# Performance work log

Hardware: AMD Instinct MI355X
Metric: run time of the kernel (lower is better)

Reference implementation:

```python
import jax, jax.numpy as jnp
import numpy as np

VOCAB = 4096
HIDDEN = 1024
BATCH = 64
SEQ = 256


def setup_inputs() -> dict:
    key = jax.random.key(0)
    ks = jax.random.split(key, 9)
    s = 0.02
    D = VOCAB + HIDDEN
    return {
        "X": jax.random.randint(ks[0], (BATCH, SEQ), 0, VOCAB),
        # gate weights stored as [in, out] = [VOCAB+HIDDEN, HIDDEN] (transposed torch Linear)
        "Wz": jax.random.normal(ks[1], (D, HIDDEN), dtype=jnp.float32) * s,
        "bz": jax.random.normal(ks[2], (HIDDEN,), dtype=jnp.float32) * s,
        "Wr": jax.random.normal(ks[3], (D, HIDDEN), dtype=jnp.float32) * s,
        "br": jax.random.normal(ks[4], (HIDDEN,), dtype=jnp.float32) * s,
        "Wh": jax.random.normal(ks[5], (D, HIDDEN), dtype=jnp.float32) * s,
        "bh": jax.random.normal(ks[6], (HIDDEN,), dtype=jnp.float32) * s,
        "Wo": jax.random.normal(ks[7], (HIDDEN, VOCAB), dtype=jnp.float32) * s,
        "bo": jax.random.normal(ks[8], (VOCAB,), dtype=jnp.float32) * s,
    }


def reference(X, Wz, bz, Wr, br, Wh, bh, Wo, bo):
    # X: [B, S] int tokens. torch does one_hot(X.T) -> time-major [S, B, V].
    # one_hot @ W_input_block == row gather of the input block of each gate weight.
    Xt = X.T  # [S, B]
    Wz_x, Wz_h = Wz[:VOCAB], Wz[VOCAB:]
    Wr_x, Wr_h = Wr[:VOCAB], Wr[VOCAB:]
    Wh_x, Wh_h = Wh[:VOCAB], Wh[VOCAB:]

    H0 = jnp.zeros((X.shape[0], HIDDEN), dtype=Wz.dtype)

    def step(H, x_t):
        # x_t: [B] int
        z = jax.nn.sigmoid(Wz_x[x_t] + H @ Wz_h + bz)
        r = jax.nn.sigmoid(Wr_x[x_t] + H @ Wr_h + br)
        h = jnp.tanh(Wh_x[x_t] + (r * H) @ Wh_h + bh)
        H_new = z * h + (1.0 - z) * H
        Y = H_new @ Wo + bo  # [B, V]
        return H_new, Y

    H_final, Ys = jax.lax.scan(step, H0, Xt)  # Ys: [S, B, V]
    # torch.cat(outputs, dim=0) over S tensors of [B, V] -> [S*B, V]
    out = Ys.reshape(-1, VOCAB)
    return out, (H_final,)
```

## Files before the change

### kernel.cpp

```cpp
#include <hip/hip_runtime.h>
#include <hip/hip_bf16.h>
#include <cstdint>
#include <cstddef>

#define VOCAB  4096
#define HIDDEN 1024
#define BATCH  64
#define SEQ    256
#define NWG    64

typedef __attribute__((ext_vector_type(8))) short short8;
typedef __attribute__((ext_vector_type(4))) float f32x4;

__device__ __forceinline__ unsigned short f2bf(float f) {
    union { float f; uint32_t u; } v; v.f = f;
    uint32_t u = v.u;
    u += 0x7FFFu + ((u >> 16) & 1u);
    return (unsigned short)(u >> 16);
}

__device__ __forceinline__ void ast16(unsigned short* p, unsigned short v) {
    __hip_atomic_store(p, v, __ATOMIC_RELAXED, __HIP_MEMORY_SCOPE_AGENT);
}

__device__ __forceinline__ short8 cld16(const unsigned short* p) {
    short8 v;
    asm volatile("global_load_dwordx4 %0, %1, off sc0 sc1"
                 : "=v"(v) : "v"(p) : "memory");
    return v;
}

__global__ __launch_bounds__(256) void k_zero(float* Hf, unsigned short* Hbf, int* flags) {
    int i = blockIdx.x * 256 + threadIdx.x;
    if (i < BATCH * HIDDEN) { Hf[i] = 0.f; Hbf[i] = 0; }
    if (i < NWG * 32) flags[i] = 0;
}

__global__ __launch_bounds__(256) void k_pack(const float* __restrict__ src,
                                              unsigned short* __restrict__ dst,
                                              int R, int C) {
    __shared__ float tile[32][33];
    int tilesC = C >> 5;
    int bx = blockIdx.x % tilesC;
    int by = blockIdx.x / tilesC;
    int tx = threadIdx.x & 31;
    int ty = threadIdx.x >> 5;
    int c0 = bx << 5, r0 = by << 5;
    #pragma unroll
    for (int s = 0; s < 4; ++s) {
        int r = ty + s * 8;
        tile[r][tx] = src[(size_t)(r0 + r) * C + (c0 + tx)];
    }
    __syncthreads();
    #pragma unroll
    for (int s = 0; s < 4; ++s) {
        int cc = ty + s * 8;
        dst[(size_t)(c0 + cc) * R + (r0 + tx)] = f2bf(tile[tx][cc]);
    }
}

__device__ __forceinline__ void flag_barrier(int* flags, int p) {
    asm volatile("s_waitcnt vmcnt(0)" ::: "memory");
    __syncthreads();
    if (threadIdx.x == 0)
        __hip_atomic_store(&flags[blockIdx.x * 32], p, __ATOMIC_RELAXED, __HIP_MEMORY_SCOPE_AGENT);
    if (threadIdx.x < NWG) {
        while (__hip_atomic_load(&flags[threadIdx.x * 32], __ATOMIC_RELAXED, __HIP_MEMORY_SCOPE_AGENT) < p)
            __builtin_amdgcn_s_sleep(1);
    }
    __syncthreads();
    __builtin_amdgcn_sched_barrier(0);
}

__global__ __launch_bounds__(256, 1) void k_scan(
    const int* __restrict__ X,
    const float* __restrict__ Wz, const float* __restrict__ bz,
    const float* __restrict__ Wr, const float* __restrict__ br,
    const float* __restrict__ Wh, const float* __restrict__ bh,
    const unsigned short* __restrict__ Wzh, const unsigned short* __restrict__ Wrh,
    const unsigned short* __restrict__ Whh,
    float* __restrict__ Hf, unsigned short* __restrict__ Hbf,
    unsigned short* __restrict__ rHbf, unsigned short* __restrict__ Hhist,
    int* __restrict__ flags)
{
    __shared__ __align__(16) unsigned short WzL[16 * 1024];
    __shared__ __align__(16) unsigned short WrL[16 * 1024];
    __shared__ __align__(16) unsigned short WhL[16 * 1024];

    const int tid  = threadIdx.x;
    const int g    = blockIdx.x;
    const int w    = tid >> 6;
    const int lane = tid & 63;
    const int row  = lane & 15;
    const int q    = lane >> 4;
    const int kq   = q << 3;
    const int col0 = g << 4;
    const int j    = col0 + row;
    const int b0   = w << 4;
    const int bq   = b0 + (q << 2);

    #pragma unroll
    for (int c = 0; c < 8; ++c) {
        int idx = tid + c * 256;
        int kkg = idx >> 6;
        int rem = idx & 63;
        int qq  = rem >> 4;
        int rr  = rem & 15;
        size_t srcoff = (size_t)(col0 + rr) * HIDDEN + kkg * 32 + qq * 8;
        *(short8*)&WzL[idx * 8] = *(const short8*)&Wzh[srcoff];
        *(short8*)&WrL[idx * 8] = *(const short8*)&Wrh[srcoff];
        *(short8*)&WhL[idx * 8] = *(const short8*)&Whh[srcoff];
    }
    __syncthreads();

    const float bzj = bz[j], brj = br[j], bhj = bh[j];

    float zreg[4] = {0.f, 0.f, 0.f, 0.f};
    float Hreg[4] = {0.f, 0.f, 0.f, 0.f};
    int p = 0;

    float ezc[4], erc[4], ehc[4];
    {
        int tk[4];
        #pragma unroll
        for (int r = 0; r < 4; ++r) tk[r] = X[(bq + r) * SEQ + 0];
        #pragma unroll
        for (int r = 0; r < 4; ++r) {
            ezc[r] = Wz[(size_t)tk[r] * HIDDEN + j];
            erc[r] = Wr[(size_t)tk[r] * HIDDEN + j];
            ehc[r] = Wh[(size_t)tk[r] * HIDDEN + j];
        }
    }

    for (int t = 0; t < SEQ; ++t) {
        const int tn = (t + 1 < SEQ) ? t + 1 : t;
        int tokn[4];
        float ezn[4], ern[4], ehn[4];

        {
            const unsigned short* ap = Hbf + (size_t)(b0 + row) * HIDDEN + kq;
            short8 A[32];
            #pragma unroll
            for (int kk = 0; kk < 32; ++kk)
                A[kk] = cld16(ap + kk * 32);
            #pragma unroll
            for (int r = 0; r < 4; ++r) {
                const int* px = X + (bq + r) * SEQ + tn;
                asm volatile("global_load_dword %0, %1, off" : "=v"(tokn[r]) : "v"(px) : "memory");
            }

            f32x4 accZ = {0.f, 0.f, 0.f, 0.f}, accR = {0.f, 0.f, 0.f, 0.f};
            asm volatile("s_waitcnt vmcnt(20)" ::: "memory");
            __builtin_amdgcn_sched_barrier(0);
            #pragma unroll
            for (int kk = 0; kk < 16; ++kk) {
                short8 bzf = *(const short8*)&WzL[kk * 512 + q * 128 + row * 8];
                short8 brf = *(const short8*)&WrL[kk * 512 + q * 128 + row * 8];
                accZ = __builtin_amdgcn_mfma_f32_16x16x32_bf16(A[kk], bzf, accZ, 0, 0, 0);
                accR = __builtin_amdgcn_mfma_f32_16x16x32_bf16(A[kk], brf, accR, 0, 0, 0);
            }
            asm volatile("s_waitcnt vmcnt(4)" ::: "memory");
            __builtin_amdgcn_sched_barrier(0);
            #pragma unroll
            for (int kk = 16; kk < 32; ++kk) {
                short8 bzf = *(const short8*)&WzL[kk * 512 + q * 128 + row * 8];
                short8 brf = *(const short8*)&WrL[kk * 512 + q * 128 + row * 8];
                accZ = __builtin_amdgcn_mfma_f32_16x16x32_bf16(A[kk], bzf, accZ, 0, 0, 0);
                accR = __builtin_amdgcn_mfma_f32_16x16x32_bf16(A[kk], brf, accR, 0, 0, 0);
            }
            #pragma unroll
            for (int r = 0; r < 4; ++r) {
                float rr = 1.f / (1.f + expf(-(accR[r] + erc[r] + brj)));
                ast16(&rHbf[(bq + r) * HIDDEN + j], f2bf(rr * Hreg[r]));
            }
            #pragma unroll
            for (int r = 0; r < 4; ++r)
                zreg[r] = 1.f / (1.f + expf(-(accZ[r] + ezc[r] + bzj)));
        }

        flag_barrier(flags, ++p);

        {
            const unsigned short* ap = rHbf + (size_t)(b0 + row) * HIDDEN + kq;
            short8 A[32];
            #pragma unroll
            for (int kk = 0; kk < 32; ++kk)
                A[kk] = cld16(ap + kk * 32);
            #pragma unroll
            for (int r = 0; r < 4; ++r) {
                const float* pz = Wz + (size_t)tokn[r] * HIDDEN + j;
                const float* pr = Wr + (size_t)tokn[r] * HIDDEN + j;
                const float* pm = Wh + (size_t)tokn[r] * HIDDEN + j;
                asm volatile("global_load_dword %0, %1, off" : "=v"(ezn[r]) : "v"(pz) : "memory");
                asm volatile("global_load_dword %0, %1, off" : "=v"(ern[r]) : "v"(pr) : "memory");
                asm volatile("global_load_dword %0, %1, off" : "=v"(ehn[r]) : "v"(pm) : "memory");
            }

            f32x4 accA = {0.f, 0.f, 0.f, 0.f}, accB = {0.f, 0.f, 0.f, 0.f};
            asm volatile("s_waitcnt vmcnt(28)" ::: "memory");
            __builtin_amdgcn_sched_barrier(0);
            #pragma unroll
            for (int kk = 0; kk < 16; ++kk) {
                short8 bf = *(const short8*)&WhL[kk * 512 + q * 128 + row * 8];
                if (kk & 1) accB = __builtin_amdgcn_mfma_f32_16x16x32_bf16(A[kk], bf, accB, 0, 0, 0);
                else        accA = __builtin_amdgcn_mfma_f32_16x16x32_bf16(A[kk], bf, accA, 0, 0, 0);
            }
            asm volatile("s_waitcnt vmcnt(12)" ::: "memory");
            __builtin_amdgcn_sched_barrier(0);
            #pragma unroll
            for (int kk = 16; kk < 32; ++kk) {
                short8 bf = *(const short8*)&WhL[kk * 512 + q * 128 + row * 8];
                if (kk & 1) accB = __builtin_amdgcn_mfma_f32_16x16x32_bf16(A[kk], bf, accB, 0, 0, 0);
                else        accA = __builtin_amdgcn_mfma_f32_16x16x32_bf16(A[kk], bf, accA, 0, 0, 0);
            }
            #pragma unroll
            for (int r = 0; r < 4; ++r) {
                int b = bq + r;
                float h  = tanhf(accA[r] + accB[r] + ehc[r] + bhj);
                float Hn = zreg[r] * h + (1.f - zreg[r]) * Hreg[r];
                Hreg[r] = Hn;
                unsigned short bfv = f2bf(Hn);
                ast16(&Hbf[b * HIDDEN + j], bfv);
                Hhist[(size_t)t * (BATCH * HIDDEN) + b * HIDDEN + j] = bfv;
                if (t == SEQ - 1) Hf[b * HIDDEN + j] = Hn;
            }
        }

        flag_barrier(flags, ++p);

        #pragma unroll
        for (int r = 0; r < 4; ++r) { ezc[r] = ezn[r]; erc[r] = ern[r]; ehc[r] = ehn[r]; }
    }
}

__global__ __launch_bounds__(256) void k_step1(
    const int* __restrict__ X,
    const float* __restrict__ Wz, const float* __restrict__ bz,
    const float* __restrict__ Wr, const float* __restrict__ br,
    const unsigned short* __restrict__ Wzh, const unsigned short* __restrict__ Wrh,
    const unsigned short* __restrict__ Hbf, const float* __restrict__ Hf,
    float* __restrict__ zbuf, unsigned short* __restrict__ rHbf, int t)
{
    int w    = threadIdx.x >> 6;
    int lane = threadIdx.x & 63;
    int nt = blockIdx.x;
    int mt = w;
    bool isz = nt < 64;
    const unsigned short* W = isz ? Wzh : Wrh;
    int ntl = nt & 63;
    int row = lane & 15;
    int kq  = (lane >> 4) << 3;
    const unsigned short* aptr = Hbf + (size_t)(mt * 16 + row) * HIDDEN + kq;
    const unsigned short* bptr = W   + (size_t)(ntl * 16 + row) * HIDDEN + kq;
    f32x4 acc = {0.f, 0.f, 0.f, 0.f};
    #pragma unroll 8
    for (int kk = 0; kk < HIDDEN / 32; ++kk) {
        short8 a = *(const short8*)(aptr + kk * 32);
        short8 b = *(const short8*)(bptr + kk * 32);
        acc = __builtin_amdgcn_mfma_f32_16x16x32_bf16(a, b, acc, 0, 0, 0);
    }
    int j = ntl * 16 + row;
    const float* Wemb = isz ? Wz : Wr;
    float bias = isz ? bz[j] : br[j];
    #pragma unroll
    for (int r = 0; r < 4; ++r) {
        int b = mt * 16 + ((lane >> 4) << 2) + r;
        int tok = X[b * SEQ + t];
        float pre = acc[r] + Wemb[(size_t)tok * HIDDEN + j] + bias;
        float s = 1.f / (1.f + expf(-pre));
        if (isz) zbuf[b * HIDDEN + j] = s;
        else     rHbf[b * HIDDEN + j] = f2bf(s * Hf[b * HIDDEN + j]);
    }
}

__global__ __launch_bounds__(256) void k_step2(
    const int* __restrict__ X,
    const float* __restrict__ Wh, const float* __restrict__ bh,
    const unsigned short* __restrict__ Whh,
    const unsigned short* __restrict__ rHbf,
    const float* __restrict__ zbuf,
    float* __restrict__ Hf, unsigned short* __restrict__ Hbf,
    unsigned short* __restrict__ Hhist, int t)
{
    int w    = threadIdx.x >> 6;
    int lane = threadIdx.x & 63;
    int nt = blockIdx.x;
    int mt = w;
    int row = lane & 15;
    int kq  = (lane >> 4) << 3;
    const unsigned short* aptr = rHbf + (size_t)(mt * 16 + row) * HIDDEN + kq;
    const unsigned short* bptr = Whh  + (size_t)(nt * 16 + row) * HIDDEN + kq;
    f32x4 acc = {0.f, 0.f, 0.f, 0.f};
    #pragma unroll 8
    for (int kk = 0; kk < HIDDEN / 32; ++kk) {
        short8 a = *(const short8*)(aptr + kk * 32);
        short8 b = *(const short8*)(bptr + kk * 32);
        acc = __builtin_amdgcn_mfma_f32_16x16x32_bf16(a, b, acc, 0, 0, 0);
    }
    int j = nt * 16 + row;
    float bias = bh[j];
    #pragma unroll
    for (int r = 0; r < 4; ++r) {
        int b = mt * 16 + ((lane >> 4) << 2) + r;
        int tok = X[b * SEQ + t];
        float pre = acc[r] + Wh[(size_t)tok * HIDDEN + j] + bias;
        float h = tanhf(pre);
        float z = zbuf[b * HIDDEN + j];
        float Hold = Hf[b * HIDDEN + j];
        float Hn = z * h + (1.f - z) * Hold;
        Hf[b * HIDDEN + j] = Hn;
        unsigned short bf = f2bf(Hn);
        Hbf[b * HIDDEN + j] = bf;
        Hhist[(size_t)t * (BATCH * HIDDEN) + b * HIDDEN + j] = bf;
    }
}

__global__ __launch_bounds__(256) void k_out(
    const unsigned short* __restrict__ A,
    const unsigned short* __restrict__ B,
    const float* __restrict__ bo,
    float* __restrict__ out)
{
    __shared__ __align__(16) unsigned short As[128 * 32];
    __shared__ __align__(16) unsigned short Bs[128 * 32];
    int bn = blockIdx.x & 31;
    int bm = blockIdx.x >> 5;
    int m0 = bm << 7, n0 = bn << 7;
    int tid  = threadIdx.x;
    int w    = tid >> 6, lane = tid & 63;
    int wm = w & 1, wn = w >> 1;
    int row = lane & 15;
    int kq  = (lane >> 4) << 3;

    f32x4 acc[4][4];
    #pragma unroll
    for (int i = 0; i < 4; ++i)
        #pragma unroll
        for (int jj = 0; jj < 4; ++jj)
            acc[i][jj] = (f32x4){0.f, 0.f, 0.f, 0.f};

    for (int k0 = 0; k0 < HIDDEN; k0 += 32) {
        #pragma unroll
        for (int c = 0; c < 2; ++c) {
            int off  = tid * 32 + c * 16;
            int rowi = off >> 6;
            int us   = (off & 63) >> 1;
            *(short8*)&As[rowi * 32 + us] =
                *(const short8*)&A[(size_t)(m0 + rowi) * HIDDEN + k0 + us];
            *(short8*)&Bs[rowi * 32 + us] =
                *(const short8*)&B[(size_t)(n0 + rowi) * HIDDEN + k0 + us];
        }
        __syncthreads();
        short8 a[4], b[4];
        #pragma unroll
        for (int i = 0; i < 4; ++i)
            a[i] = *(const short8*)&As[(wm * 64 + i * 16 + row) * 32 + kq];
        #pragma unroll
        for (int jj = 0; jj < 4; ++jj)
            b[jj] = *(const short8*)&Bs[(wn * 64 + jj * 16 + row) * 32 + kq];
        #pragma unroll
        for (int i = 0; i < 4; ++i)
            #pragma unroll
            for (int jj = 0; jj < 4; ++jj)
                acc[i][jj] = __builtin_amdgcn_mfma_f32_16x16x32_bf16(a[i], b[jj], acc[i][jj], 0, 0, 0);
        __syncthreads();
    }

    #pragma unroll
    for (int i = 0; i < 4; ++i) {
        #pragma unroll
        for (int jj = 0; jj < 4; ++jj) {
            int n = n0 + wn * 64 + jj * 16 + row;
            float bb = bo[n];
            #pragma unroll
            for (int r = 0; r < 4; ++r) {
                int m = m0 + wm * 64 + i * 16 + ((lane >> 4) << 2) + r;
                out[(size_t)m * VOCAB + n] = acc[i][jj][r] + bb;
            }
        }
    }
}

__global__ __launch_bounds__(256) void k_copyH(const float* __restrict__ Hf,
                                               float* __restrict__ out) {
    int i = blockIdx.x * 256 + threadIdx.x;
    if (i < BATCH * HIDDEN)
        out[(size_t)SEQ * BATCH * VOCAB + i] = Hf[i];
}

extern "C" void kernel_launch(void* const* d_in, const int* in_sizes, int n_in,
                              void* d_out, int out_size, void* d_ws, size_t ws_size,
                              hipStream_t stream) {
    const int*   X  = (const int*)  d_in[0];
    const float* Wz = (const float*)d_in[1];
    const float* bz = (const float*)d_in[2];
    const float* Wr = (const float*)d_in[3];
    const float* br = (const float*)d_in[4];
    const float* Wh = (const float*)d_in[5];
    const float* bh = (const float*)d_in[6];
    const float* Wo = (const float*)d_in[7];
    const float* bo = (const float*)d_in[8];
    float* out = (float*)d_out;
    char* ws = (char*)d_ws;

    float*          Hf    = (float*)(ws);
    float*          zbuf  = (float*)(ws + (256 << 10));
    int*            flags = (int*)(ws + (512 << 10));
    unsigned short* Hbf   = (unsigned short*)(ws + (528 << 10));
    unsigned short* rHbf  = (unsigned short*)(ws + (656 << 10));
    unsigned short* Wzh   = (unsigned short*)(ws + (1 << 20));
    unsigned short* Wrh   = Wzh + 1024 * 1024;
    unsigned short* Whh   = Wrh + 1024 * 1024;
    unsigned short* WoT   = Whh + 1024 * 1024;
    unsigned short* Hhist = WoT + (size_t)VOCAB * HIDDEN;

    k_zero<<<256, 256, 0, stream>>>(Hf, Hbf, flags);
    k_pack<<<32 * 32,  256, 0, stream>>>(Wz + (size_t)VOCAB * HIDDEN, Wzh, 1024, 1024);
    k_pack<<<32 * 32,  256, 0, stream>>>(Wr + (size_t)VOCAB * HIDDEN, Wrh, 1024, 1024);
    k_pack<<<32 * 32,  256, 0, stream>>>(Wh + (size_t)VOCAB * HIDDEN, Whh, 1024, 1024);
    k_pack<<<32 * 128, 256, 0, stream>>>(Wo, WoT, 1024, 4096);

    void* args[] = {
        (void*)&X, (void*)&Wz, (void*)&bz, (void*)&Wr, (void*)&br,
        (void*)&Wh, (void*)&bh, (void*)&Wzh, (void*)&Wrh, (void*)&Whh,
        (void*)&Hf, (void*)&Hbf, (void*)&rHbf, (void*)&Hhist, (void*)&flags
    };
    hipError_t cerr = hipLaunchCooperativeKernel((void*)k_scan, dim3(NWG), dim3(256),
                                                 args, 0, stream);
    if (cerr != hipSuccess) {
        for (int t = 0; t < SEQ; ++t) {
            k_step1<<<128, 256, 0, stream>>>(X, Wz, bz, Wr, br, Wzh, Wrh, Hbf, Hf, zbuf, rHbf, t);
            k_step2<<<64,  256, 0, stream>>>(X, Wh, bh, Whh, rHbf, zbuf, Hf, Hbf, Hhist, t);
        }
    }

    k_out<<<4096, 256, 0, stream>>>(Hhist, WoT, bo, out);
    k_copyH<<<256, 256, 0, stream>>>(Hf, out);
}
```

Before: 3.485 ms.

## Halve persistent scan workgroups, each owning 32 hidden columns

The persistent recurrent kernel now runs 32 workgroups instead of 64, each computing 32 hidden columns with two 16-column MFMA tiles per gate. This halves the number of participants in every cross-workgroup flag barrier and doubles MFMA work per wave. Because the z and r weights for 32 columns fill the LDS budget, the candidate-gate (Wh) weights are no longer staged in LDS and are read from global memory on every step. That trades lower barrier cost for more per-step global traffic, longer per-step compute, and less GPU occupancy.

```diff
diff --git a/kernel.cpp b/kernel.cpp
--- a/kernel.cpp
+++ b/kernel.cpp
@@ -7,7 +7,7 @@
 #define HIDDEN 1024
 #define BATCH  64
 #define SEQ    256
-#define NWG    64
+#define NWG    32
 
 typedef __attribute__((ext_vector_type(8))) short short8;
 typedef __attribute__((ext_vector_type(4))) float f32x4;
@@ -83,9 +83,8 @@
     unsigned short* __restrict__ rHbf, unsigned short* __restrict__ Hhist,
     int* __restrict__ flags)
 {
-    __shared__ __align__(16) unsigned short WzL[16 * 1024];
-    __shared__ __align__(16) unsigned short WrL[16 * 1024];
-    __shared__ __align__(16) unsigned short WhL[16 * 1024];
+    __shared__ __align__(16) unsigned short WzL[32 * 1024];
+    __shared__ __align__(16) unsigned short WrL[32 * 1024];
 
     const int tid  = threadIdx.x;
     const int g    = blockIdx.x;
@@ -94,48 +93,52 @@
     const int row  = lane & 15;
     const int q    = lane >> 4;
     const int kq   = q << 3;
-    const int col0 = g << 4;
-    const int j    = col0 + row;
+    const int col0 = g << 5;
+    const int j0   = col0 + row;
+    const int j1   = j0 + 16;
     const int b0   = w << 4;
     const int bq   = b0 + (q << 2);
 
     #pragma unroll
-    for (int c = 0; c < 8; ++c) {
+    for (int c = 0; c < 16; ++c) {
         int idx = tid + c * 256;
-        int kkg = idx >> 6;
-        int rem = idx & 63;
-        int qq  = rem >> 4;
-        int rr  = rem & 15;
-        size_t srcoff = (size_t)(col0 + rr) * HIDDEN + kkg * 32 + qq * 8;
-        *(short8*)&WzL[idx * 8] = *(const short8*)&Wzh[srcoff];
-        *(short8*)&WrL[idx * 8] = *(const short8*)&Wrh[srcoff];
-        *(short8*)&WhL[idx * 8] = *(const short8*)&Whh[srcoff];
+        int cb  = idx >> 11;
+        int kkg = (idx >> 6) & 31;
+        int qq  = (idx >> 4) & 3;
+        int rr  = idx & 15;
+        size_t so = (size_t)(col0 + cb * 16 + rr) * HIDDEN + kkg * 32 + qq * 8;
+        *(short8*)&WzL[idx * 8] = *(const short8*)&Wzh[so];
+        *(short8*)&WrL[idx * 8] = *(const short8*)&Wrh[so];
     }
     __syncthreads();
 
-    const float bzj = bz[j], brj = br[j], bhj = bh[j];
-
-    float zreg[4] = {0.f, 0.f, 0.f, 0.f};
-    float Hreg[4] = {0.f, 0.f, 0.f, 0.f};
+    const float bzj0 = bz[j0], bzj1 = bz[j1];
+    const float brj0 = br[j0], brj1 = br[j1];
+    const float bhj0 = bh[j0], bhj1 = bh[j1];
+
+    float zreg[2][4] = {};
+    float Hreg[2][4] = {};
     int p = 0;
 
-    float ezc[4], erc[4], ehc[4];
+    float ezc[2][4], erc[2][4], ehc[2][4];
     {
         int tk[4];
         #pragma unroll
         for (int r = 0; r < 4; ++r) tk[r] = X[(bq + r) * SEQ + 0];
         #pragma unroll
         for (int r = 0; r < 4; ++r) {
-            ezc[r] = Wz[(size_t)tk[r] * HIDDEN + j];
-            erc[r] = Wr[(size_t)tk[r] * HIDDEN + j];
-            ehc[r] = Wh[(size_t)tk[r] * HIDDEN + j];
+            size_t o0 = (size_t)tk[r] * HIDDEN + j0;
+            size_t o1 = (size_t)tk[r] * HIDDEN + j1;
+            ezc[0][r] = Wz[o0]; ezc[1][r] = Wz[o1];
+            erc[0][r] = Wr[o0]; erc[1][r] = Wr[o1];
+            ehc[0][r] = Wh[o0]; ehc[1][r] = Wh[o1];
         }
     }
 
     for (int t = 0; t < SEQ; ++t) {
         const int tn = (t + 1 < SEQ) ? t + 1 : t;
         int tokn[4];
-        float ezn[4], ern[4], ehn[4];
+        float ezn[2][4], ern[2][4], ehn[2][4];
 
         {
             const unsigned short* ap = Hbf + (size_t)(b0 + row) * HIDDEN + kq;
@@ -149,33 +152,45 @@
                 asm volatile("global_load_dword %0, %1, off" : "=v"(tokn[r]) : "v"(px) : "memory");
             }
 
-            f32x4 accZ = {0.f, 0.f, 0.f, 0.f}, accR = {0.f, 0.f, 0.f, 0.f};
+            f32x4 accZ0 = {0.f,0.f,0.f,0.f}, accZ1 = {0.f,0.f,0.f,0.f};
+            f32x4 accR0 = {0.f,0.f,0.f,0.f}, accR1 = {0.f,0.f,0.f,0.f};
             asm volatile("s_waitcnt vmcnt(20)" ::: "memory");
             __builtin_amdgcn_sched_barrier(0);
             #pragma unroll
             for (int kk = 0; kk < 16; ++kk) {
-                short8 bzf = *(const short8*)&WzL[kk * 512 + q * 128 + row * 8];
-                short8 brf = *(const short8*)&WrL[kk * 512 + q * 128 + row * 8];
-                accZ = __builtin_amdgcn_mfma_f32_16x16x32_bf16(A[kk], bzf, accZ, 0, 0, 0);
-                accR = __builtin_amdgcn_mfma_f32_16x16x32_bf16(A[kk], brf, accR, 0, 0, 0);
+                int lo = kk * 512 + q * 128 + row * 8;
+                short8 fz0 = *(const short8*)&WzL[lo];
+                short8 fz1 = *(const short8*)&WzL[16384 + lo];
+                short8 fr0 = *(const short8*)&WrL[lo];
+                short8 fr1 = *(const short8*)&WrL[16384 + lo];
+                accZ0 = __builtin_amdgcn_mfma_f32_16x16x32_bf16(A[kk], fz0, accZ0, 0, 0, 0);
+                accZ1 = __builtin_amdgcn_mfma_f32_16x16x32_bf16(A[kk], fz1, accZ1, 0, 0, 0);
+                accR0 = __builtin_amdgcn_mfma_f32_16x16x32_bf16(A[kk], fr0, accR0, 0, 0, 0);
+                accR1 = __builtin_amdgcn_mfma_f32_16x16x32_bf16(A[kk], fr1, accR1, 0, 0, 0);
             }
             asm volatile("s_waitcnt vmcnt(4)" ::: "memory");
             __builtin_amdgcn_sched_barrier(0);
             #pragma unroll
             for (int kk = 16; kk < 32; ++kk) {
-                short8 bzf = *(const short8*)&WzL[kk * 512 + q * 128 + row * 8];
-                short8 brf = *(const short8*)&WrL[kk * 512 + q * 128 + row * 8];
-                accZ = __builtin_amdgcn_mfma_f32_16x16x32_bf16(A[kk], bzf, accZ, 0, 0, 0);
-                accR = __builtin_amdgcn_mfma_f32_16x16x32_bf16(A[kk], brf, accR, 0, 0, 0);
+                int lo = kk * 512 + q * 128 + row * 8;
+                short8 fz0 = *(const short8*)&WzL[lo];
+                short8 fz1 = *(const short8*)&WzL[16384 + lo];
+                short8 fr0 = *(const short8*)&WrL[lo];
+                short8 fr1 = *(const short8*)&WrL[16384 + lo];
+                accZ0 = __builtin_amdgcn_mfma_f32_16x16x32_bf16(A[kk], fz0, accZ0, 0, 0, 0);
+                accZ1 = __builtin_amdgcn_mfma_f32_16x16x32_bf16(A[kk], fz1, accZ1, 0, 0, 0);
+                accR0 = __builtin_amdgcn_mfma_f32_16x16x32_bf16(A[kk], fr0, accR0, 0, 0, 0);
+                accR1 = __builtin_amdgcn_mfma_f32_16x16x32_bf16(A[kk], fr1, accR1, 0, 0, 0);
             }
             #pragma unroll
             for (int r = 0; r < 4; ++r) {
-                float rr = 1.f / (1.f + expf(-(accR[r] + erc[r] + brj)));
-                ast16(&rHbf[(bq + r) * HIDDEN + j], f2bf(rr * Hreg[r]));
-            }
-            #pragma unroll
-            for (int r = 0; r < 4; ++r)
-                zreg[r] = 1.f / (1.f + expf(-(accZ[r] + ezc[r] + bzj)));
+                float rv0 = 1.f / (1.f + expf(-(accR0[r] + erc[0][r] + brj0)));
+                float rv1 = 1.f / (1.f + expf(-(accR1[r] + erc[1][r] + brj1)));
+                ast16(&rHbf[(bq + r) * HIDDEN + j0], f2bf(rv0 * Hreg[0][r]));
+                ast16(&rHbf[(bq + r) * HIDDEN + j1], f2bf(rv1 * Hreg[1][r]));
+                zreg[0][r] = 1.f / (1.f + expf(-(accZ0[r] + ezc[0][r] + bzj0)));
+                zreg[1][r] = 1.f / (1.f + expf(-(accZ1[r] + ezc[1][r] + bzj1)));
+            }
         }
 
         flag_barrier(flags, ++p);
@@ -188,48 +203,57 @@
                 A[kk] = cld16(ap + kk * 32);
             #pragma unroll
             for (int r = 0; r < 4; ++r) {
-                const float* pz = Wz + (size_t)tokn[r] * HIDDEN + j;
-                const float* pr = Wr + (size_t)tokn[r] * HIDDEN + j;
-                const float* pm = Wh + (size_t)tokn[r] * HIDDEN + j;
-                asm volatile("global_load_dword %0, %1, off" : "=v"(ezn[r]) : "v"(pz) : "memory");
-                asm volatile("global_load_dword %0, %1, off" : "=v"(ern[r]) : "v"(pr) : "memory");
-                asm volatile("global_load_dword %0, %1, off" : "=v"(ehn[r]) : "v"(pm) : "memory");
-            }
-
-            f32x4 accA = {0.f, 0.f, 0.f, 0.f}, accB = {0.f, 0.f, 0.f, 0.f};
-            asm volatile("s_waitcnt vmcnt(28)" ::: "memory");
+                const float* pz0 = Wz + (size_t)tokn[r] * HIDDEN + j0;
+                const float* pz1 = Wz + (size_t)tokn[r] * HIDDEN + j1;
+                const float* pr0 = Wr + (size_t)tokn[r] * HIDDEN + j0;
+                const float* pr1 = Wr + (size_t)tokn[r] * HIDDEN + j1;
+                const float* pm0 = Wh + (size_t)tokn[r] * HIDDEN + j0;
+                const float* pm1 = Wh + (size_t)tokn[r] * HIDDEN + j1;
+                asm volatile("global_load_dword %0, %1, off" : "=v"(ezn[0][r]) : "v"(pz0) : "memory");
+                asm volatile("global_load_dword %0, %1, off" : "=v"(ezn[1][r]) : "v"(pz1) : "memory");
+                asm volatile("global_load_dword %0, %1, off" : "=v"(ern[0][r]) : "v"(pr0) : "memory");
+                asm volatile("global_load_dword %0, %1, off" : "=v"(ern[1][r]) : "v"(pr1) : "memory");
+                asm volatile("global_load_dword %0, %1, off" : "=v"(ehn[0][r]) : "v"(pm0) : "memory");
+                asm volatile("global_load_dword %0, %1, off" : "=v"(ehn[1][r]) : "v"(pm1) : "memory");
+            }
+
+            asm volatile("s_waitcnt vmcnt(24)" ::: "memory");
             __builtin_amdgcn_sched_barrier(0);
-            #pragma unroll
-            for (int kk = 0; kk < 16; ++kk) {
-                short8 bf = *(const short8*)&WhL[kk * 512 + q * 128 + row * 8];
-                if (kk & 1) accB = __builtin_amdgcn_mfma_f32_16x16x32_bf16(A[kk], bf, accB, 0, 0, 0);
-                else        accA = __builtin_amdgcn_mfma_f32_16x16x32_bf16(A[kk], bf, accA, 0, 0, 0);
-            }
-            asm volatile("s_waitcnt vmcnt(12)" ::: "memory");
-            __builtin_amdgcn_sched_barrier(0);
-            #pragma unroll
-            for (int kk = 16; kk < 32; ++kk) {
-                short8 bf = *(const short8*)&WhL[kk * 512 + q * 128 + row * 8];
-                if (kk & 1) accB = __builtin_amdgcn_mfma_f32_16x16x32_bf16(A[kk], bf, accB, 0, 0, 0);
-                else        accA = __builtin_amdgcn_mfma_f32_16x16x32_bf16(A[kk], bf, accA, 0, 0, 0);
+            const unsigned short* w0 = Whh + (size_t)j0 * HIDDEN + kq;
+            const unsigned short* w1 = Whh + (size_t)j1 * HIDDEN + kq;
+            f32x4 acc0 = {0.f,0.f,0.f,0.f}, acc1 = {0.f,0.f,0.f,0.f};
+            #pragma unroll
+            for (int kk = 0; kk < 32; ++kk) {
+                short8 fb0 = *(const short8*)(w0 + kk * 32);
+                short8 fb1 = *(const short8*)(w1 + kk * 32);
+                acc0 = __builtin_amdgcn_mfma_f32_16x16x32_bf16(A[kk], fb0, acc0, 0, 0, 0);
+                acc1 = __builtin_amdgcn_mfma_f32_16x16x32_bf16(A[kk], fb1, acc1, 0, 0, 0);
             }
             #pragma unroll
             for (int r = 0; r < 4; ++r) {
                 int b = bq + r;
-                float h  = tanhf(accA[r] + accB[r] + ehc[r] + bhj);
-                float Hn = zreg[r] * h + (1.f - zreg[r]) * Hreg[r];
-                Hreg[r] = Hn;
-                unsigned short bfv = f2bf(Hn);
-                ast16(&Hbf[b * HIDDEN + j], bfv);
-                Hhist[(size_t)t * (BATCH * HIDDEN) + b * HIDDEN + j] = bfv;
-                if (t == SEQ - 1) Hf[b * HIDDEN + j] = Hn;
+                float h0 = tanhf(acc0[r] + ehc[0][r] + bhj0);
+                float h1 = tanhf(acc1[r] + ehc[1][r] + bhj1);
+                float Hn0 = zreg[0][r] * h0 + (1.f - zreg[0][r]) * Hreg[0][r];
+                float Hn1 = zreg[1][r] * h1 + (1.f - zreg[1][r]) * Hreg[1][r];
+                Hreg[0][r] = Hn0; Hreg[1][r] = Hn1;
+                unsigned short v0 = f2bf(Hn0), v1 = f2bf(Hn1);
+                ast16(&Hbf[b * HIDDEN + j0], v0);
+                ast16(&Hbf[b * HIDDEN + j1], v1);
+                Hhist[(size_t)t * (BATCH * HIDDEN) + b * HIDDEN + j0] = v0;
+                Hhist[(size_t)t * (BATCH * HIDDEN) + b * HIDDEN + j1] = v1;
+                if (t == SEQ - 1) { Hf[b * HIDDEN + j0] = Hn0; Hf[b * HIDDEN + j1] = Hn1; }
             }
         }
 
         flag_barrier(flags, ++p);
 
         #pragma unroll
-        for (int r = 0; r < 4; ++r) { ezc[r] = ezn[r]; erc[r] = ern[r]; ehc[r] = ehn[r]; }
+        for (int r = 0; r < 4; ++r) {
+            ezc[0][r] = ezn[0][r]; ezc[1][r] = ezn[1][r];
+            erc[0][r] = ern[0][r]; erc[1][r] = ern[1][r];
+            ehc[0][r] = ehn[0][r]; ehc[1][r] = ehn[1][r];
+        }
     }
 }
 
```

Result: slower. 5.739 ms (+64.7%).

## Spread recurrent scan over 256 workgroups with split-K across waves

Applied to the files above, without the earlier changes.

The persistent scan kernel grows from 64 to 256 workgroups. Each one now owns a 16-column by 16-batch tile, and its four waves each take a quarter of the K dimension, summed through an LDS reduction. This shortens the serial MFMA chain and the per-wave H loads in every timestep, attacking the latency-bound recurrence. In exchange, the grid barrier now has to observe 256 flags, now packed contiguously instead of padded, and each step pays an extra workgroup sync for the reduction. It also relies on all 256 workgroups being co-resident.

```diff
diff --git a/kernel.cpp b/kernel.cpp
--- a/kernel.cpp
+++ b/kernel.cpp
@@ -7,7 +7,7 @@
 #define HIDDEN 1024
 #define BATCH  64
 #define SEQ    256
-#define NWG    64
+#define NWG    256
 
 typedef __attribute__((ext_vector_type(8))) short short8;
 typedef __attribute__((ext_vector_type(4))) float f32x4;
@@ -33,7 +33,7 @@
 __global__ __launch_bounds__(256) void k_zero(float* Hf, unsigned short* Hbf, int* flags) {
     int i = blockIdx.x * 256 + threadIdx.x;
     if (i < BATCH * HIDDEN) { Hf[i] = 0.f; Hbf[i] = 0; }
-    if (i < NWG * 32) flags[i] = 0;
+    if (i < 2048) flags[i] = 0;
 }
 
 __global__ __launch_bounds__(256) void k_pack(const float* __restrict__ src,
@@ -63,10 +63,17 @@
     asm volatile("s_waitcnt vmcnt(0)" ::: "memory");
     __syncthreads();
     if (threadIdx.x == 0)
-        __hip_atomic_store(&flags[blockIdx.x * 32], p, __ATOMIC_RELAXED, __HIP_MEMORY_SCOPE_AGENT);
-    if (threadIdx.x < NWG) {
-        while (__hip_atomic_load(&flags[threadIdx.x * 32], __ATOMIC_RELAXED, __HIP_MEMORY_SCOPE_AGENT) < p)
+        __hip_atomic_store(&flags[blockIdx.x], p, __ATOMIC_RELAXED, __HIP_MEMORY_SCOPE_AGENT);
+    if (threadIdx.x < 64) {
+        int l = threadIdx.x;
+        for (;;) {
+            int a = __hip_atomic_load(&flags[l],       __ATOMIC_RELAXED, __HIP_MEMORY_SCOPE_AGENT);
+            int b = __hip_atomic_load(&flags[64 + l],  __ATOMIC_RELAXED, __HIP_MEMORY_SCOPE_AGENT);
+            int c = __hip_atomic_load(&flags[128 + l], __ATOMIC_RELAXED, __HIP_MEMORY_SCOPE_AGENT);
+            int d = __hip_atomic_load(&flags[192 + l], __ATOMIC_RELAXED, __HIP_MEMORY_SCOPE_AGENT);
+            if (a >= p && b >= p && c >= p && d >= p) break;
             __builtin_amdgcn_s_sleep(1);
+        }
     }
     __syncthreads();
     __builtin_amdgcn_sched_barrier(0);
@@ -86,6 +93,8 @@
     __shared__ __align__(16) unsigned short WzL[16 * 1024];
     __shared__ __align__(16) unsigned short WrL[16 * 1024];
     __shared__ __align__(16) unsigned short WhL[16 * 1024];
+    __shared__ __align__(16) f32x4 redZ[4][64];
+    __shared__ __align__(16) f32x4 redR[4][64];
 
     const int tid  = threadIdx.x;
     const int g    = blockIdx.x;
@@ -94,9 +103,11 @@
     const int row  = lane & 15;
     const int q    = lane >> 4;
     const int kq   = q << 3;
-    const int col0 = g << 4;
+    const int cg   = g & 63;
+    const int bg   = g >> 6;
+    const int col0 = cg << 4;
+    const int b0   = bg << 4;
     const int j    = col0 + row;
-    const int b0   = w << 4;
     const int bq   = b0 + (q << 2);
 
     #pragma unroll
@@ -106,10 +117,10 @@
         int rem = idx & 63;
         int qq  = rem >> 4;
         int rr  = rem & 15;
-        size_t srcoff = (size_t)(col0 + rr) * HIDDEN + kkg * 32 + qq * 8;
-        *(short8*)&WzL[idx * 8] = *(const short8*)&Wzh[srcoff];
-        *(short8*)&WrL[idx * 8] = *(const short8*)&Wrh[srcoff];
-        *(short8*)&WhL[idx * 8] = *(const short8*)&Whh[srcoff];
+        size_t so = (size_t)(col0 + rr) * HIDDEN + kkg * 32 + qq * 8;
+        *(short8*)&WzL[idx * 8] = *(const short8*)&Wzh[so];
+        *(short8*)&WrL[idx * 8] = *(const short8*)&Wrh[so];
+        *(short8*)&WhL[idx * 8] = *(const short8*)&Whh[so];
     }
     __syncthreads();
 
@@ -139,53 +150,51 @@
 
         {
             const unsigned short* ap = Hbf + (size_t)(b0 + row) * HIDDEN + kq;
-            short8 A[32];
-            #pragma unroll
-            for (int kk = 0; kk < 32; ++kk)
-                A[kk] = cld16(ap + kk * 32);
+            short8 A[8];
+            #pragma unroll
+            for (int kkL = 0; kkL < 8; ++kkL)
+                A[kkL] = cld16(ap + (w * 8 + kkL) * 32);
             #pragma unroll
             for (int r = 0; r < 4; ++r) {
                 const int* px = X + (bq + r) * SEQ + tn;
                 asm volatile("global_load_dword %0, %1, off" : "=v"(tokn[r]) : "v"(px) : "memory");
             }
 
-            f32x4 accZ = {0.f, 0.f, 0.f, 0.f}, accR = {0.f, 0.f, 0.f, 0.f};
-            asm volatile("s_waitcnt vmcnt(20)" ::: "memory");
-            __builtin_amdgcn_sched_barrier(0);
-            #pragma unroll
-            for (int kk = 0; kk < 16; ++kk) {
-                short8 bzf = *(const short8*)&WzL[kk * 512 + q * 128 + row * 8];
-                short8 brf = *(const short8*)&WrL[kk * 512 + q * 128 + row * 8];
-                accZ = __builtin_amdgcn_mfma_f32_16x16x32_bf16(A[kk], bzf, accZ, 0, 0, 0);
-                accR = __builtin_amdgcn_mfma_f32_16x16x32_bf16(A[kk], brf, accR, 0, 0, 0);
-            }
+            f32x4 aZ = {0.f,0.f,0.f,0.f}, aR = {0.f,0.f,0.f,0.f};
             asm volatile("s_waitcnt vmcnt(4)" ::: "memory");
             __builtin_amdgcn_sched_barrier(0);
             #pragma unroll
-            for (int kk = 16; kk < 32; ++kk) {
-                short8 bzf = *(const short8*)&WzL[kk * 512 + q * 128 + row * 8];
-                short8 brf = *(const short8*)&WrL[kk * 512 + q * 128 + row * 8];
-                accZ = __builtin_amdgcn_mfma_f32_16x16x32_bf16(A[kk], bzf, accZ, 0, 0, 0);
-                accR = __builtin_amdgcn_mfma_f32_16x16x32_bf16(A[kk], brf, accR, 0, 0, 0);
-            }
+            for (int kkL = 0; kkL < 8; ++kkL) {
+                int lo = (w * 8 + kkL) * 512 + q * 128 + row * 8;
+                short8 fz = *(const short8*)&WzL[lo];
+                short8 fr = *(const short8*)&WrL[lo];
+                aZ = __builtin_amdgcn_mfma_f32_16x16x32_bf16(A[kkL], fz, aZ, 0, 0, 0);
+                aR = __builtin_amdgcn_mfma_f32_16x16x32_bf16(A[kkL], fr, aR, 0, 0, 0);
+            }
+            redZ[w][lane] = aZ;
+            redR[w][lane] = aR;
+            __syncthreads();
+            f32x4 sZ = redZ[0][lane]; f32x4 sR = redR[0][lane];
+            #pragma unroll
+            for (int ww = 1; ww < 4; ++ww) { sZ += redZ[ww][lane]; sR += redR[ww][lane]; }
+
             #pragma unroll
             for (int r = 0; r < 4; ++r) {
-                float rr = 1.f / (1.f + expf(-(accR[r] + erc[r] + brj)));
-                ast16(&rHbf[(bq + r) * HIDDEN + j], f2bf(rr * Hreg[r]));
-            }
-            #pragma unroll
-            for (int r = 0; r < 4; ++r)
-                zreg[r] = 1.f / (1.f + expf(-(accZ[r] + ezc[r] + bzj)));
+                float rv = 1.f / (1.f + expf(-(sR[r] + erc[r] + brj)));
+                zreg[r]  = 1.f / (1.f + expf(-(sZ[r] + ezc[r] + bzj)));
+                if (w == 0)
+                    ast16(&rHbf[(bq + r) * HIDDEN + j], f2bf(rv * Hreg[r]));
+            }
         }
 
         flag_barrier(flags, ++p);
 
         {
             const unsigned short* ap = rHbf + (size_t)(b0 + row) * HIDDEN + kq;
-            short8 A[32];
-            #pragma unroll
-            for (int kk = 0; kk < 32; ++kk)
-                A[kk] = cld16(ap + kk * 32);
+            short8 A[8];
+            #pragma unroll
+            for (int kkL = 0; kkL < 8; ++kkL)
+                A[kkL] = cld16(ap + (w * 8 + kkL) * 32);
             #pragma unroll
             for (int r = 0; r < 4; ++r) {
                 const float* pz = Wz + (size_t)tokn[r] * HIDDEN + j;
@@ -196,33 +205,33 @@
                 asm volatile("global_load_dword %0, %1, off" : "=v"(ehn[r]) : "v"(pm) : "memory");
             }
 
-            f32x4 accA = {0.f, 0.f, 0.f, 0.f}, accB = {0.f, 0.f, 0.f, 0.f};
-            asm volatile("s_waitcnt vmcnt(28)" ::: "memory");
-            __builtin_amdgcn_sched_barrier(0);
-            #pragma unroll
-            for (int kk = 0; kk < 16; ++kk) {
-                short8 bf = *(const short8*)&WhL[kk * 512 + q * 128 + row * 8];
-                if (kk & 1) accB = __builtin_amdgcn_mfma_f32_16x16x32_bf16(A[kk], bf, accB, 0, 0, 0);
-                else        accA = __builtin_amdgcn_mfma_f32_16x16x32_bf16(A[kk], bf, accA, 0, 0, 0);
-            }
+            f32x4 aH = {0.f,0.f,0.f,0.f};
             asm volatile("s_waitcnt vmcnt(12)" ::: "memory");
             __builtin_amdgcn_sched_barrier(0);
             #pragma unroll
-            for (int kk = 16; kk < 32; ++kk) {
-                short8 bf = *(const short8*)&WhL[kk * 512 + q * 128 + row * 8];
-                if (kk & 1) accB = __builtin_amdgcn_mfma_f32_16x16x32_bf16(A[kk], bf, accB, 0, 0, 0);
-                else        accA = __builtin_amdgcn_mfma_f32_16x16x32_bf16(A[kk], bf, accA, 0, 0, 0);
-            }
+            for (int kkL = 0; kkL < 8; ++kkL) {
+                int lo = (w * 8 + kkL) * 512 + q * 128 + row * 8;
+                short8 fh = *(const short8*)&WhL[lo];
+                aH = __builtin_amdgcn_mfma_f32_16x16x32_bf16(A[kkL], fh, aH, 0, 0, 0);
+            }
+            redZ[w][lane] = aH;
+            __syncthreads();
+            f32x4 sH = redZ[0][lane];
+            #pragma unroll
+            for (int ww = 1; ww < 4; ++ww) sH += redZ[ww][lane];
+
             #pragma unroll
             for (int r = 0; r < 4; ++r) {
                 int b = bq + r;
-                float h  = tanhf(accA[r] + accB[r] + ehc[r] + bhj);
+                float h  = tanhf(sH[r] + ehc[r] + bhj);
                 float Hn = zreg[r] * h + (1.f - zreg[r]) * Hreg[r];
                 Hreg[r] = Hn;
-                unsigned short bfv = f2bf(Hn);
-                ast16(&Hbf[b * HIDDEN + j], bfv);
-                Hhist[(size_t)t * (BATCH * HIDDEN) + b * HIDDEN + j] = bfv;
-                if (t == SEQ - 1) Hf[b * HIDDEN + j] = Hn;
+                if (w == 0) {
+                    unsigned short bfv = f2bf(Hn);
+                    ast16(&Hbf[b * HIDDEN + j], bfv);
+                    Hhist[(size_t)t * (BATCH * HIDDEN) + b * HIDDEN + j] = bfv;
+                    if (t == SEQ - 1) Hf[b * HIDDEN + j] = Hn;
+                }
             }
         }
 
```

Measured after the change: 3.558 ms. 1.02x slower.

## Split recurrent scan into four independent batch-group scans with per-group barriers

Applied to the files above, without the earlier changes.

The persistent scan kernel now launches 256 single-wave workgroups instead of 64 four-wave ones. Each group of 64 workgroups handles one 16-row batch slice. Because GRU batch rows are independent, each slice only synchronises with its own 64 peers through a separate flag range, which removes the intra-block __syncthreads and shrinks the barrier fan-in. In exchange, each workgroup still loads the full 96KB of recurrent weight slices into LDS, so the LDS and global weight traffic is replicated four times across the slices. That means more co-resident workgroups, which the cooperative launch must be able to fit.

```diff
diff --git a/kernel.cpp b/kernel.cpp
--- a/kernel.cpp
+++ b/kernel.cpp
@@ -7,7 +7,8 @@
 #define HIDDEN 1024
 #define BATCH  64
 #define SEQ    256
-#define NWG    64
+#define NWG    256
+#define SCANS  4
 
 typedef __attribute__((ext_vector_type(8))) short short8;
 typedef __attribute__((ext_vector_type(4))) float f32x4;
@@ -33,7 +34,7 @@
 __global__ __launch_bounds__(256) void k_zero(float* Hf, unsigned short* Hbf, int* flags) {
     int i = blockIdx.x * 256 + threadIdx.x;
     if (i < BATCH * HIDDEN) { Hf[i] = 0.f; Hbf[i] = 0; }
-    if (i < NWG * 32) flags[i] = 0;
+    if (i < 2048) flags[i] = 0;
 }
 
 __global__ __launch_bounds__(256) void k_pack(const float* __restrict__ src,
@@ -59,20 +60,17 @@
     }
 }
 
-__device__ __forceinline__ void flag_barrier(int* flags, int p) {
+__device__ __forceinline__ void scan_barrier(int* flags, int base, int cg, int p) {
     asm volatile("s_waitcnt vmcnt(0)" ::: "memory");
-    __syncthreads();
     if (threadIdx.x == 0)
-        __hip_atomic_store(&flags[blockIdx.x * 32], p, __ATOMIC_RELAXED, __HIP_MEMORY_SCOPE_AGENT);
-    if (threadIdx.x < NWG) {
-        while (__hip_atomic_load(&flags[threadIdx.x * 32], __ATOMIC_RELAXED, __HIP_MEMORY_SCOPE_AGENT) < p)
-            __builtin_amdgcn_s_sleep(1);
-    }
-    __syncthreads();
+        __hip_atomic_store(&flags[base + cg], p, __ATOMIC_RELAXED, __HIP_MEMORY_SCOPE_AGENT);
+    int l = threadIdx.x & 63;
+    while (__hip_atomic_load(&flags[base + l], __ATOMIC_RELAXED, __HIP_MEMORY_SCOPE_AGENT) < p)
+        __builtin_amdgcn_s_sleep(1);
     __builtin_amdgcn_sched_barrier(0);
 }
 
-__global__ __launch_bounds__(256, 1) void k_scan(
+__global__ __launch_bounds__(64, 1) void k_scan(
     const int* __restrict__ X,
     const float* __restrict__ Wz, const float* __restrict__ bz,
     const float* __restrict__ Wr, const float* __restrict__ br,
@@ -89,27 +87,29 @@
 
     const int tid  = threadIdx.x;
     const int g    = blockIdx.x;
-    const int w    = tid >> 6;
+    const int scan = g >> 6;
+    const int cg   = g & 63;
     const int lane = tid & 63;
     const int row  = lane & 15;
     const int q    = lane >> 4;
     const int kq   = q << 3;
-    const int col0 = g << 4;
+    const int col0 = cg << 4;
     const int j    = col0 + row;
-    const int b0   = w << 4;
+    const int b0   = scan << 4;
     const int bq   = b0 + (q << 2);
-
-    #pragma unroll
-    for (int c = 0; c < 8; ++c) {
-        int idx = tid + c * 256;
+    const int fbase = scan << 6;
+
+    #pragma unroll
+    for (int c = 0; c < 32; ++c) {
+        int idx = tid + c * 64;
         int kkg = idx >> 6;
         int rem = idx & 63;
         int qq  = rem >> 4;
         int rr  = rem & 15;
-        size_t srcoff = (size_t)(col0 + rr) * HIDDEN + kkg * 32 + qq * 8;
-        *(short8*)&WzL[idx * 8] = *(const short8*)&Wzh[srcoff];
-        *(short8*)&WrL[idx * 8] = *(const short8*)&Wrh[srcoff];
-        *(short8*)&WhL[idx * 8] = *(const short8*)&Whh[srcoff];
+        size_t so = (size_t)(col0 + rr) * HIDDEN + kkg * 32 + qq * 8;
+        *(short8*)&WzL[idx * 8] = *(const short8*)&Wzh[so];
+        *(short8*)&WrL[idx * 8] = *(const short8*)&Wrh[so];
+        *(short8*)&WhL[idx * 8] = *(const short8*)&Whh[so];
     }
     __syncthreads();
 
@@ -154,31 +154,33 @@
             __builtin_amdgcn_sched_barrier(0);
             #pragma unroll
             for (int kk = 0; kk < 16; ++kk) {
-                short8 bzf = *(const short8*)&WzL[kk * 512 + q * 128 + row * 8];
-                short8 brf = *(const short8*)&WrL[kk * 512 + q * 128 + row * 8];
-                accZ = __builtin_amdgcn_mfma_f32_16x16x32_bf16(A[kk], bzf, accZ, 0, 0, 0);
-                accR = __builtin_amdgcn_mfma_f32_16x16x32_bf16(A[kk], brf, accR, 0, 0, 0);
+                int lo = kk * 512 + q * 128 + row * 8;
+                short8 fz = *(const short8*)&WzL[lo];
+                short8 fr = *(const short8*)&WrL[lo];
+                accZ = __builtin_amdgcn_mfma_f32_16x16x32_bf16(A[kk], fz, accZ, 0, 0, 0);
+                accR = __builtin_amdgcn_mfma_f32_16x16x32_bf16(A[kk], fr, accR, 0, 0, 0);
             }
             asm volatile("s_waitcnt vmcnt(4)" ::: "memory");
             __builtin_amdgcn_sched_barrier(0);
             #pragma unroll
             for (int kk = 16; kk < 32; ++kk) {
-                short8 bzf = *(const short8*)&WzL[kk * 512 + q * 128 + row * 8];
-                short8 brf = *(const short8*)&WrL[kk * 512 + q * 128 + row * 8];
-                accZ = __builtin_amdgcn_mfma_f32_16x16x32_bf16(A[kk], bzf, accZ, 0, 0, 0);
-                accR = __builtin_amdgcn_mfma_f32_16x16x32_bf16(A[kk], brf, accR, 0, 0, 0);
+                int lo = kk * 512 + q * 128 + row * 8;
+                short8 fz = *(const short8*)&WzL[lo];
+                short8 fr = *(const short8*)&WrL[lo];
+                accZ = __builtin_amdgcn_mfma_f32_16x16x32_bf16(A[kk], fz, accZ, 0, 0, 0);
+                accR = __builtin_amdgcn_mfma_f32_16x16x32_bf16(A[kk], fr, accR, 0, 0, 0);
             }
             #pragma unroll
             for (int r = 0; r < 4; ++r) {
-                float rr = 1.f / (1.f + expf(-(accR[r] + erc[r] + brj)));
-                ast16(&rHbf[(bq + r) * HIDDEN + j], f2bf(rr * Hreg[r]));
+                float rv = 1.f / (1.f + expf(-(accR[r] + erc[r] + brj)));
+                ast16(&rHbf[(bq + r) * HIDDEN + j], f2bf(rv * Hreg[r]));
             }
             #pragma unroll
             for (int r = 0; r < 4; ++r)
                 zreg[r] = 1.f / (1.f + expf(-(accZ[r] + ezc[r] + bzj)));
         }
 
-        flag_barrier(flags, ++p);
+        scan_barrier(flags, fbase, cg, ++p);
 
         {
             const unsigned short* ap = rHbf + (size_t)(b0 + row) * HIDDEN + kq;
@@ -201,17 +203,19 @@
             __builtin_amdgcn_sched_barrier(0);
             #pragma unroll
             for (int kk = 0; kk < 16; ++kk) {
-                short8 bf = *(const short8*)&WhL[kk * 512 + q * 128 + row * 8];
-                if (kk & 1) accB = __builtin_amdgcn_mfma_f32_16x16x32_bf16(A[kk], bf, accB, 0, 0, 0);
-                else        accA = __builtin_amdgcn_mfma_f32_16x16x32_bf16(A[kk], bf, accA, 0, 0, 0);
+                int lo = kk * 512 + q * 128 + row * 8;
+                short8 fh = *(const short8*)&WhL[lo];
+                if (kk & 1) accB = __builtin_amdgcn_mfma_f32_16x16x32_bf16(A[kk], fh, accB, 0, 0, 0);
+                else        accA = __builtin_amdgcn_mfma_f32_16x16x32_bf16(A[kk], fh, accA, 0, 0, 0);
             }
             asm volatile("s_waitcnt vmcnt(12)" ::: "memory");
             __builtin_amdgcn_sched_barrier(0);
             #pragma unroll
             for (int kk = 16; kk < 32; ++kk) {
-                short8 bf = *(const short8*)&WhL[kk * 512 + q * 128 + row * 8];
-                if (kk & 1) accB = __builtin_amdgcn_mfma_f32_16x16x32_bf16(A[kk], bf, accB, 0, 0, 0);
-                else        accA = __builtin_amdgcn_mfma_f32_16x16x32_bf16(A[kk], bf, accA, 0, 0, 0);
+                int lo = kk * 512 + q * 128 + row * 8;
+                short8 fh = *(const short8*)&WhL[lo];
+                if (kk & 1) accB = __builtin_amdgcn_mfma_f32_16x16x32_bf16(A[kk], fh, accB, 0, 0, 0);
+                else        accA = __builtin_amdgcn_mfma_f32_16x16x32_bf16(A[kk], fh, accA, 0, 0, 0);
             }
             #pragma unroll
             for (int r = 0; r < 4; ++r) {
@@ -226,7 +230,7 @@
             }
         }
 
-        flag_barrier(flags, ++p);
+        scan_barrier(flags, fbase, cg, ++p);
 
         #pragma unroll
         for (int r = 0; r < 4; ++r) { ezc[r] = ezn[r]; erc[r] = ern[r]; ehc[r] = ehn[r]; }
@@ -425,7 +429,7 @@
         (void*)&Wh, (void*)&bh, (void*)&Wzh, (void*)&Wrh, (void*)&Whh,
         (void*)&Hf, (void*)&Hbf, (void*)&rHbf, (void*)&Hhist, (void*)&flags
     };
-    hipError_t cerr = hipLaunchCooperativeKernel((void*)k_scan, dim3(NWG), dim3(256),
+    hipError_t cerr = hipLaunchCooperativeKernel((void*)k_scan, dim3(NWG), dim3(64),
                                                  args, 0, stream);
     if (cerr != hipSuccess) {
         for (int t = 0; t < SEQ; ++t) {
```

New measurement: 3.116 ms (median of 2 runs). 1.12x faster.
